# Performance work log

Hardware: AMD Instinct MI355X
Metric: run time of the kernel (lower is better)

Reference implementation:

```python
import jax, jax.numpy as jnp
import numpy as np

DIM = 256
HEADS = 8
HEAD_DIM = DIM // HEADS
B = 4
Wd, Hd = 48, 48
N = Wd * Hd  # 2304


def _layernorm(x, g, b, eps=1e-5):
    mu = jnp.mean(x, axis=-1, keepdims=True)
    var = jnp.mean(jnp.square(x - mu), axis=-1, keepdims=True)
    return (x - mu) * jax.lax.rsqrt(var + eps) * g + b


def _build_mask(mask):
    # Binarize: <1 -> 0, >0 -> 1 (identity on {0,1} inputs)
    m = (mask > 0).astype(jnp.float32)
    flat = m.reshape(B, m.shape[1], Hd * Wd)[:, 0, :]  # [B, N]
    # mask[b,i,j] zeroed where (flat[j]==0 & flat[i]==1) | (flat[j]==0 & flat[i]==0)
    col0 = flat[:, None, :] == 0   # varies along j
    row = flat[:, :, None]         # varies along i
    bad = (col0 & (row == 1)) | (col0 & (row == 0))
    return (~bad).astype(jnp.float32)  # [B, N, N]


def setup_inputs() -> dict:
    key = jax.random.key(0)
    ks = jax.random.split(key, 12)
    s = 0.02
    x = jax.random.normal(ks[0], (B, N, DIM), jnp.float32)
    mask = jax.random.randint(ks[1], (B, 1, Wd, Hd), 0, 2).astype(jnp.float32)
    inp = {
        "x": x,
        "mask": mask,
        "ln_g": jnp.ones((DIM,), jnp.float32),
        "ln_b": jnp.zeros((DIM,), jnp.float32),
        "Wq": jax.random.normal(ks[2], (DIM, DIM), jnp.float32) * s,
        "bq": jnp.zeros((DIM,), jnp.float32),
        "Wk": jax.random.normal(ks[3], (DIM, DIM), jnp.float32) * s,
        "bk": jnp.zeros((DIM,), jnp.float32),
        "Wv": jax.random.normal(ks[4], (DIM, DIM), jnp.float32) * s,
        "bv": jnp.zeros((DIM,), jnp.float32),
        "Wp": jax.random.normal(ks[5], (DIM, DIM), jnp.float32) * s,
        "bp": jnp.zeros((DIM,), jnp.float32),
    }
    return inp


def reference(x, mask, ln_g, ln_b, Wq, bq, Wk, bk, Wv, bv, Wp, bp):
    Bx, Nx, C = x.shape
    mask_f = _build_mask(mask)  # [B, N, N]
    xn = _layernorm(x, ln_g, ln_b)
    def heads(Wm, bm):
        return (xn @ Wm + bm).reshape(Bx, Nx, HEADS, HEAD_DIM).transpose(0, 2, 1, 3)
    q = heads(Wq, bq)
    k = heads(Wk, bk)
    v = heads(Wv, bv)
    # NOTE: no 1/sqrt(d) scaling in the original; multiplicative 0/1 mask pre-softmax
    attn = jnp.einsum("bhnd,bhmd->bhnm", q, k) * mask_f[:, None, :, :]
    attn = jax.nn.softmax(attn, axis=-1)
    out = jnp.einsum("bhnm,bhmd->bhnd", attn, v)
    out = out.transpose(0, 2, 1, 3).reshape(Bx, Nx, C)
    return out @ Wp + bp
```

## Files before the change

kernel.cpp:

```cpp
#include <hip/hip_runtime.h>
#include <math.h>

typedef __attribute__((ext_vector_type(8))) short short8;
typedef __attribute__((ext_vector_type(4))) float f32x4;

constexpr int B   = 4;
constexpr int N   = 2304;
constexpr int DIM = 256;
constexpr int NH  = 8;
constexpr int DH  = 32;
constexpr int M   = B * N;
constexpr int SLOTS = 2336;
constexpr int CST = SLOTS * DH;
constexpr int XPB = SLOTS * DIM;

__device__ inline unsigned short f2bf(float f) {
    union { float f; unsigned u; } c; c.f = f;
    unsigned u = c.u;
    u += 0x7fffu + ((u >> 16) & 1u);
    return (unsigned short)(u >> 16);
}
__device__ inline unsigned short f2bf_trunc(float f) {
    union { float f; unsigned u; } c; c.f = f;
    return (unsigned short)(c.u >> 16);
}
__device__ inline float bf2f(unsigned short h) {
    union { unsigned u; float f; } c; c.u = ((unsigned)h) << 16;
    return c.f;
}

__device__ inline size_t fo256(int r, int k) {
    return ((size_t)((r >> 4) * 8 + (k >> 5)) << 9)
         + (size_t)(((((k & 31) >> 3) << 4) + (r & 15)) * 8 + (k & 7));
}
__device__ inline size_t foQK(int n, int d) {
    return ((size_t)(n >> 4) << 9)
         + (size_t)((((d >> 3) << 4) + (n & 15)) * 8 + (d & 7));
}
__device__ inline size_t foVTC(int d, int key) {
    return ((size_t)((d >> 4) * (SLOTS / 32) + (key >> 5)) << 9)
         + (size_t)(((((key & 31) >> 3) << 4) + (d & 15)) * 8 + (key & 7));
}

__global__ __launch_bounds__(256) void mask_scan(
    const float* __restrict__ mask, int* __restrict__ inv,
    int* __restrict__ ncp, float* __restrict__ vm)
{
    __shared__ int wsum[4];
    int b = blockIdx.x, t = threadIdx.x;
    int wave = t >> 6, lane = t & 63;
    vm[b * 256 + t] = 0.f;
    int cnt = 0;
    for (int j = t; j < N; j += 256) cnt += (mask[(size_t)b * N + j] > 0.f);
    #pragma unroll
    for (int o = 32; o > 0; o >>= 1) cnt += __shfl_down(cnt, o, 64);
    if (lane == 0) wsum[wave] = cnt;
    __syncthreads();
    int Nc = wsum[0] + wsum[1] + wsum[2] + wsum[3];
    int Nkp = (Nc + 31) & ~31;
    if (t == 0) { ncp[b * 2] = Nc; ncp[b * 2 + 1] = Nkp; }
    int baseK = 0;
    for (int j0 = 0; j0 < N; j0 += 256) {
        int j = j0 + t;
        bool keep = mask[(size_t)b * N + j] > 0.f;
        unsigned long long bal = __ballot(keep);
        int pos = __popcll(bal & ((1ull << lane) - 1ull));
        int wc  = __popcll(bal);
        __syncthreads();
        if (lane == 0) wsum[wave] = wc;
        __syncthreads();
        int wb = 0;
        for (int w = 0; w < wave; ++w) wb += wsum[w];
        int tot = wsum[0] + wsum[1] + wsum[2] + wsum[3];
        int keptBefore = baseK + wb + pos;
        if (keep) inv[(size_t)b * SLOTS + keptBefore] = j;
        else      inv[(size_t)b * SLOTS + Nkp + (j - keptBefore)] = j;
        baseK += tot;
    }
}

__global__ __launch_bounds__(256) void ln_kernel(
    const float* __restrict__ x, const float* __restrict__ g,
    const float* __restrict__ bta,
    unsigned short* __restrict__ xh, unsigned short* __restrict__ xl)
{
    int tid = threadIdx.x;
    int wave = tid >> 6, lane = tid & 63;
    int row = blockIdx.x * 4 + wave;
    float4 v = *(const float4*)&x[(size_t)row * DIM + lane * 4];
    float s = v.x + v.y + v.z + v.w;
    #pragma unroll
    for (int o = 32; o > 0; o >>= 1) s += __shfl_xor(s, o, 64);
    float mu = s * (1.0f / DIM);
    float d0 = v.x - mu, d1 = v.y - mu, d2 = v.z - mu, d3 = v.w - mu;
    float s2 = d0 * d0 + d1 * d1 + d2 * d2 + d3 * d3;
    #pragma unroll
    for (int o = 32; o > 0; o >>= 1) s2 += __shfl_xor(s2, o, 64);
    float r = rsqrtf(s2 * (1.0f / DIM) + 1e-5f);
    float4 gg = *(const float4*)&g[lane * 4];
    float4 bb = *(const float4*)&bta[lane * 4];
    float y0 = d0 * r * gg.x + bb.x;
    float y1 = d1 * r * gg.y + bb.y;
    float y2 = d2 * r * gg.z + bb.z;
    float y3 = d3 * r * gg.w + bb.w;
    ushort4 hi, lo;
    hi.x = f2bf(y0); lo.x = f2bf(y0 - bf2f(hi.x));
    hi.y = f2bf(y1); lo.y = f2bf(y1 - bf2f(hi.y));
    hi.z = f2bf(y2); lo.z = f2bf(y2 - bf2f(hi.z));
    hi.w = f2bf(y3); lo.w = f2bf(y3 - bf2f(hi.w));
    size_t o = fo256(row, lane * 4);
    *(ushort4*)&xh[o] = hi;
    *(ushort4*)&xl[o] = lo;
}

__global__ __launch_bounds__(256) void split_w(
    const float* __restrict__ Wq, const float* __restrict__ Wk,
    const float* __restrict__ Wv, const float* __restrict__ Wp,
    unsigned short* __restrict__ Wth, unsigned short* __restrict__ Wtl)
{
    int z = blockIdx.z;
    const float* W = (z == 0) ? Wq : (z == 1) ? Wk : (z == 2) ? Wv : Wp;
    unsigned short* oh = Wth + (size_t)z * DIM * DIM;
    unsigned short* ol = Wtl + (size_t)z * DIM * DIM;
    __shared__ float t[32][33];
    int tid = threadIdx.x;
    int tx = tid & 31, ty0 = tid >> 5;
    int n0 = blockIdx.x * 32, k0 = blockIdx.y * 32;
    for (int ty = ty0; ty < 32; ty += 8)
        t[ty][tx] = W[(size_t)(k0 + ty) * DIM + n0 + tx];
    __syncthreads();
    for (int nn = ty0; nn < 32; nn += 8) {
        float v = t[tx][nn];
        unsigned short hh = f2bf(v);
        size_t o = fo256(n0 + nn, k0 + tx);
        oh[o] = hh;
        ol[o] = f2bf(v - bf2f(hh));
    }
}

__global__ __launch_bounds__(256) void permute_x(
    const unsigned short* __restrict__ xh, const unsigned short* __restrict__ xl,
    const int* __restrict__ inv, const int* __restrict__ ncp,
    unsigned short* __restrict__ xph, unsigned short* __restrict__ xpl)
{
    int tid = threadIdx.x;
    int wave = tid >> 6, lane = tid & 63;
    int kq = lane >> 4, r = lane & 15;
    int rtg = blockIdx.x * 4 + wave;
    int b = rtg / (SLOTS / 16), rt = rtg % (SLOTS / 16);
    int y = blockIdx.y;
    const unsigned short* src = (y & 1) ? xl : xh;
    unsigned short* dst = ((y & 1) ? xpl : xph) + (size_t)b * XPB;
    int slot = rt * 16 + r;
    int Nc = ncp[b * 2], Nkp = ncp[b * 2 + 1];
    int mend = Nkp + (N - Nc);
    bool pad = (slot >= Nc && slot < Nkp) || slot >= mend;
    int n = pad ? -1 : inv[(size_t)b * SLOTS + slot];
    #pragma unroll
    for (int kt = 0; kt < 4; ++kt) {
        int k0 = ((y >> 1) * 4 + kt) * 32;
        short8 v = {0, 0, 0, 0, 0, 0, 0, 0};
        if (n >= 0) {
            int gn = b * N + n;
            v = *(const short8*)&src[(((size_t)(gn >> 4) * 8 + (k0 >> 5)) << 9)
                                     + (kq * 16 + (gn & 15)) * 8];
        }
        *(short8*)&dst[(((size_t)(rt * 8 + (k0 >> 5))) << 9) + lane * 8] = v;
    }
}

__global__ __launch_bounds__(256, 4) void gemm_qkv(
    const unsigned short* __restrict__ xh, const unsigned short* __restrict__ xl,
    const unsigned short* __restrict__ xph, const unsigned short* __restrict__ xpl,
    const unsigned short* __restrict__ Wth, const unsigned short* __restrict__ Wtl,
    const float* __restrict__ bq, const float* __restrict__ bk,
    const float* __restrict__ bv, const int* __restrict__ ncp,
    unsigned short* __restrict__ qb, unsigned short* __restrict__ kc,
    unsigned short* __restrict__ vc)
{
    constexpr size_t WSZ = (size_t)DIM * DIM;
    int z = blockIdx.z, bx = blockIdx.x;
    int tid = threadIdx.x;
    int wave = tid >> 6, lane = tid & 63;
    int quad = lane >> 4, l16 = lane & 15;
    const unsigned short *PAh, *PAl, *PBh, *PBl;
    int arow0, brow0, b;
    if (z == 0) {
        if (bx >= 576) return;
        arow0 = (bx >> 3) * 128 + wave * 32;
        brow0 = (bx & 7) * 32;
        b = ((bx >> 3) * 128) / N;
        PAh = xh; PAl = xl;
        PBh = Wth; PBl = Wtl;
    } else if (z == 1) {
        b = bx / 152;
        int rr = bx % 152;
        arow0 = (rr >> 3) * 128 + wave * 32;
        brow0 = (rr & 7) * 32;
        if (arow0 >= SLOTS) return;
        if (arow0 >= ncp[b * 2 + 1]) return;
        PAh = xph + (size_t)b * XPB; PAl = xpl + (size_t)b * XPB;
        PBh = Wth + WSZ; PBl = Wtl + WSZ;
    } else {
        if (bx >= 584) return;
        int nidx = bx % 292;
        b = nidx / 73;
        arow0 = (bx / 292) * 128 + wave * 32;
        brow0 = (nidx % 73) * 32;
        PAh = Wth + 2 * WSZ; PAl = Wtl + 2 * WSZ;
        PBh = xph + (size_t)b * XPB; PBl = xpl + (size_t)b * XPB;
    }
    f32x4 acc[2][2] = {};
    #pragma unroll
    for (int k0 = 0; k0 < DIM; k0 += 32) {
        size_t at = (((size_t)(arow0 >> 4) * 8 + (k0 >> 5)) << 9) + lane * 8;
        size_t bt = (((size_t)(brow0 >> 4) * 8 + (k0 >> 5)) << 9) + lane * 8;
        short8 ah0 = *(const short8*)&PAh[at];
        short8 al0 = *(const short8*)&PAl[at];
        short8 ah1 = *(const short8*)&PAh[at + 4096];
        short8 al1 = *(const short8*)&PAl[at + 4096];
        short8 bh0 = *(const short8*)&PBh[bt];
        short8 bl0 = *(const short8*)&PBl[bt];
        short8 bh1 = *(const short8*)&PBh[bt + 4096];
        short8 bl1 = *(const short8*)&PBl[bt + 4096];
        acc[0][0] = __builtin_amdgcn_mfma_f32_16x16x32_bf16(ah0, bh0, acc[0][0], 0, 0, 0);
        acc[0][0] = __builtin_amdgcn_mfma_f32_16x16x32_bf16(ah0, bl0, acc[0][0], 0, 0, 0);
        acc[0][0] = __builtin_amdgcn_mfma_f32_16x16x32_bf16(al0, bh0, acc[0][0], 0, 0, 0);
        acc[0][1] = __builtin_amdgcn_mfma_f32_16x16x32_bf16(ah0, bh1, acc[0][1], 0, 0, 0);
        acc[0][1] = __builtin_amdgcn_mfma_f32_16x16x32_bf16(ah0, bl1, acc[0][1], 0, 0, 0);
        acc[0][1] = __builtin_amdgcn_mfma_f32_16x16x32_bf16(al0, bh1, acc[0][1], 0, 0, 0);
        acc[1][0] = __builtin_amdgcn_mfma_f32_16x16x32_bf16(ah1, bh0, acc[1][0], 0, 0, 0);
        acc[1][0] = __builtin_amdgcn_mfma_f32_16x16x32_bf16(ah1, bl0, acc[1][0], 0, 0, 0);
        acc[1][0] = __builtin_amdgcn_mfma_f32_16x16x32_bf16(al1, bh0, acc[1][0], 0, 0, 0);
        acc[1][1] = __builtin_amdgcn_mfma_f32_16x16x32_bf16(ah1, bh1, acc[1][1], 0, 0, 0);
        acc[1][1] = __builtin_amdgcn_mfma_f32_16x16x32_bf16(ah1, bl1, acc[1][1], 0, 0, 0);
        acc[1][1] = __builtin_amdgcn_mfma_f32_16x16x32_bf16(al1, bh1, acc[1][1], 0, 0, 0);
    }
    if (z == 0) {
        int nbase = arow0 - b * N;
        #pragma unroll
        for (int j = 0; j < 2; ++j) {
            int c = brow0 + j * 16 + l16;
            int h = c >> 5, d = c & 31;
            float bs = bq[c];
            unsigned short* ob = qb + (size_t)(b * NH + h) * ((size_t)N * DH);
            #pragma unroll
            for (int i = 0; i < 2; ++i)
            #pragma unroll
            for (int r = 0; r < 4; ++r) {
                int n = nbase + i * 16 + quad * 4 + r;
                ob[foQK(n, d)] = f2bf(acc[i][j][r] + bs);
            }
        }
    } else if (z == 1) {
        #pragma unroll
        for (int j = 0; j < 2; ++j) {
            int c = brow0 + j * 16 + l16;
            int h = c >> 5, d = c & 31;
            float bs = bk[c];
            unsigned short* ob = kc + (size_t)(b * NH + h) * CST;
            #pragma unroll
            for (int i = 0; i < 2; ++i)
            #pragma unroll
            for (int r = 0; r < 4; ++r) {
                int slot = arow0 + i * 16 + quad * 4 + r;
                ob[foQK(slot, d)] = f2bf(acc[i][j][r] + bs);
            }
        }
    } else {
        #pragma unroll
        for (int i = 0; i < 2; ++i)
        #pragma unroll
        for (int r = 0; r < 4; ++r) {
            int m = arow0 + i * 16 + quad * 4 + r;
            int h = m >> 5, d = m & 31;
            float bs = bv[m];
            unsigned short* ob = vc + (size_t)(b * NH + h) * CST;
            #pragma unroll
            for (int j = 0; j < 2; ++j) {
                int key = brow0 + j * 16 + l16;
                ob[foVTC(d, key)] = f2bf(acc[i][j][r] + bs);
            }
        }
    }
}

__global__ __launch_bounds__(256) void vmsum_kernel(
    const unsigned short* __restrict__ vc, const int* __restrict__ ncp,
    float* __restrict__ vm)
{
    int bh = blockIdx.x, b = bh >> 3;
    int tid = threadIdx.x;
    int wave = tid >> 6, lane = tid & 63;
    int kq = lane >> 4, l16 = lane & 15;
    int Nc = ncp[b * 2], Nkp = ncp[b * 2 + 1];
    int mend = Nkp + (N - Nc);
    int tbeg = Nkp >> 5, tend = (mend + 31) >> 5;
    int wgid = blockIdx.y * 4 + wave;
    const int WSTEP = 32;
    const unsigned short* vcb = vc + (size_t)bh * CST;
    #pragma unroll
    for (int dt = 0; dt < 2; ++dt) {
        float s = 0.f;
        for (int t = tbeg + wgid; t < tend; t += WSTEP) {
            short8 v = *(const short8*)&vcb[((size_t)(dt * (SLOTS / 32) + t) << 9) + lane * 8];
            int keyb = t * 32 + kq * 8;
            #pragma unroll
            for (int j = 0; j < 8; ++j)
                s += (keyb + j >= Nkp && keyb + j < mend) ? bf2f((unsigned short)v[j]) : 0.f;
        }
        s += __shfl_xor(s, 16, 64);
        s += __shfl_xor(s, 32, 64);
        if (lane < 16) atomicAdd(&vm[bh * 32 + dt * 16 + l16], s);
    }
}

__global__ __launch_bounds__(256, 4) void attn_kernel(
    const unsigned short* __restrict__ Qb,
    const unsigned short* __restrict__ Kc,
    const unsigned short* __restrict__ Vc,
    const int* __restrict__ ncp,
    float* __restrict__ po, float* __restrict__ pl)
{
    __shared__ unsigned short pbuf[8 * 16 * 40];
    int tid  = threadIdx.x;
    int wave = tid >> 6, lane = tid & 63;
    int quad = lane >> 4, l16 = lane & 15;
    int bh = blockIdx.y, b = bh >> 3;
    int sp = blockIdx.z;
    int q0 = (blockIdx.x * 4 + wave) * 32;

    const unsigned short* Qf = Qb + (size_t)bh * ((size_t)N * DH);
    const unsigned short* Kf = Kc + (size_t)bh * CST;
    const unsigned short* Vf = Vc + (size_t)bh * CST;

    int Nc  = ncp[b * 2];
    int Nkp = ncp[b * 2 + 1];
    int chunks = Nkp >> 5;
    int cbeg = sp ? (chunks >> 1) : 0;
    int cend = sp ? chunks : (chunks >> 1);
    int kbeg = cbeg << 5, kend = cend << 5;

    short8 qA0 = *(const short8*)&Qf[((size_t)(q0 >> 4) << 9) + lane * 8];
    short8 qA1 = *(const short8*)&Qf[((size_t)((q0 >> 4) + 1) << 9) + lane * 8];

    f32x4 o00 = {0,0,0,0}, o01 = {0,0,0,0}, o10 = {0,0,0,0}, o11 = {0,0,0,0};
    float l0[4] = {0,0,0,0}, l1[4] = {0,0,0,0};

    unsigned short* pb0 = &pbuf[(wave * 2 + 0) * 640];
    unsigned short* pb1 = &pbuf[(wave * 2 + 1) * 640];

    short8 kB0 = *(const short8*)&Kf[((size_t)(kbeg >> 4) << 9) + lane * 8];
    short8 kB1 = *(const short8*)&Kf[((size_t)((kbeg >> 4) + 1) << 9) + lane * 8];
    short8 vB0 = *(const short8*)&Vf[((size_t)(kbeg >> 5) << 9) + lane * 8];
    short8 vB1 = *(const short8*)&Vf[((size_t)((SLOTS / 32) + (kbeg >> 5)) << 9) + lane * 8];

    for (int k0 = kbeg; k0 < kend; k0 += 32) {
        int kn = (k0 + 32 < kend) ? k0 + 32 : kbeg;
        short8 nk0 = *(const short8*)&Kf[((size_t)(kn >> 4) << 9) + lane * 8];
        short8 nk1 = *(const short8*)&Kf[((size_t)((kn >> 4) + 1) << 9) + lane * 8];
        short8 nv0 = *(const short8*)&Vf[((size_t)(kn >> 5) << 9) + lane * 8];
        short8 nv1 = *(const short8*)&Vf[((size_t)((SLOTS / 32) + (kn >> 5)) << 9) + lane * 8];

        bool in0 = (k0 + l16) < Nc;
        bool in1 = (k0 + 16 + l16) < Nc;
        f32x4 z = {0,0,0,0};
        f32x4 s00 = __builtin_amdgcn_mfma_f32_16x16x32_bf16(qA0, kB0, z, 0, 0, 0);
        f32x4 s01 = __builtin_amdgcn_mfma_f32_16x16x32_bf16(qA0, kB1, z, 0, 0, 0);
        f32x4 s10 = __builtin_amdgcn_mfma_f32_16x16x32_bf16(qA1, kB0, z, 0, 0, 0);
        f32x4 s11 = __builtin_amdgcn_mfma_f32_16x16x32_bf16(qA1, kB1, z, 0, 0, 0);
        #pragma unroll
        for (int r = 0; r < 4; ++r) {
            int row = quad * 4 + r;
            float p00 = in0 ? __expf(s00[r]) : 0.f;
            float p01 = in1 ? __expf(s01[r]) : 0.f;
            float p10 = in0 ? __expf(s10[r]) : 0.f;
            float p11 = in1 ? __expf(s11[r]) : 0.f;
            l0[r] += p00 + p01;
            l1[r] += p10 + p11;
            pb0[row * 40 + l16]      = f2bf_trunc(p00);
            pb0[row * 40 + 16 + l16] = f2bf_trunc(p01);
            pb1[row * 40 + l16]      = f2bf_trunc(p10);
            pb1[row * 40 + 16 + l16] = f2bf_trunc(p11);
        }
        short8 pA0 = *(const short8*)&pb0[l16 * 40 + quad * 8];
        short8 pA1 = *(const short8*)&pb1[l16 * 40 + quad * 8];
        o00 = __builtin_amdgcn_mfma_f32_16x16x32_bf16(pA0, vB0, o00, 0, 0, 0);
        o01 = __builtin_amdgcn_mfma_f32_16x16x32_bf16(pA0, vB1, o01, 0, 0, 0);
        o10 = __builtin_amdgcn_mfma_f32_16x16x32_bf16(pA1, vB0, o10, 0, 0, 0);
        o11 = __builtin_amdgcn_mfma_f32_16x16x32_bf16(pA1, vB1, o11, 0, 0, 0);

        kB0 = nk0; kB1 = nk1; vB0 = nv0; vB1 = nv1;
    }
    #pragma unroll
    for (int r = 0; r < 4; ++r) {
        #pragma unroll
        for (int off = 1; off < 16; off <<= 1) {
            l0[r] += __shfl_xor(l0[r], off, 64);
            l1[r] += __shfl_xor(l1[r], off, 64);
        }
    }
    size_t pbase = (size_t)(bh * 2 + sp) * N;
    #pragma unroll
    for (int r = 0; r < 4; ++r) {
        int row = quad * 4 + r;
        size_t b0 = (pbase + q0 + row) * DH;
        size_t b1 = (pbase + q0 + 16 + row) * DH;
        po[b0 + l16]      = o00[r];
        po[b0 + 16 + l16] = o01[r];
        po[b1 + l16]      = o10[r];
        po[b1 + 16 + l16] = o11[r];
        if (l16 == 0) {
            pl[pbase + q0 + row]      = l0[r];
            pl[pbase + q0 + 16 + row] = l1[r];
        }
    }
}

__global__ __launch_bounds__(256) void combine_kernel(
    const float* __restrict__ po, const float* __restrict__ pl,
    const float* __restrict__ vm, const int* __restrict__ ncp,
    unsigned short* __restrict__ ahn_hi, unsigned short* __restrict__ ahn_lo)
{
    int idx = blockIdx.x * 256 + threadIdx.x;
    int bhq = idx >> 2;
    int dg  = (idx & 3) * 8;
    int bh = bhq / N, q = bhq - bh * N;
    int b = bh >> 3, h = bh & 7;
    size_t p0 = ((size_t)(bh * 2 + 0) * N + q) * DH + dg;
    size_t p1 = ((size_t)(bh * 2 + 1) * N + q) * DH + dg;
    int Nc = ncp[b * 2];
    float l = pl[(size_t)(bh * 2) * N + q] + pl[(size_t)(bh * 2 + 1) * N + q]
            + (float)(N - Nc);
    float inv = 1.f / l;
    float4 a0 = *(const float4*)&po[p0];
    float4 a1 = *(const float4*)&po[p0 + 4];
    float4 c0 = *(const float4*)&po[p1];
    float4 c1 = *(const float4*)&po[p1 + 4];
    float4 m0 = *(const float4*)&vm[bh * 32 + dg];
    float4 m1 = *(const float4*)&vm[bh * 32 + dg + 4];
    float vals[8] = {
        (a0.x + c0.x + m0.x) * inv, (a0.y + c0.y + m0.y) * inv,
        (a0.z + c0.z + m0.z) * inv, (a0.w + c0.w + m0.w) * inv,
        (a1.x + c1.x + m1.x) * inv, (a1.y + c1.y + m1.y) * inv,
        (a1.z + c1.z + m1.z) * inv, (a1.w + c1.w + m1.w) * inv };
    union { unsigned short u[8]; short8 v; } hi, lo;
    #pragma unroll
    for (int j = 0; j < 8; ++j) {
        unsigned short t = f2bf(vals[j]);
        hi.u[j] = t;
        lo.u[j] = f2bf(vals[j] - bf2f(t));
    }
    size_t o = fo256(b * N + q, h * 32 + dg);
    *(short8*)&ahn_hi[o] = hi.v;
    *(short8*)&ahn_lo[o] = lo.v;
}

__global__ __launch_bounds__(256, 4) void gemm_p(
    const unsigned short* __restrict__ Ahi, const unsigned short* __restrict__ Alo,
    const unsigned short* __restrict__ Wth, const unsigned short* __restrict__ Wtl,
    const float* __restrict__ bias, float* __restrict__ out)
{
    constexpr size_t WSZ = (size_t)DIM * DIM;
    const unsigned short* Bhi = Wth + 3 * WSZ;
    const unsigned short* Blo = Wtl + 3 * WSZ;
    int tid = threadIdx.x;
    int wave = tid >> 6, lane = tid & 63;
    int quad = lane >> 4, l16 = lane & 15;
    int r0 = blockIdx.y * 128 + wave * 32;
    int c0 = blockIdx.x * 16;
    f32x4 acc0 = {}, acc1 = {};
    #pragma unroll
    for (int k0 = 0; k0 < DIM; k0 += 32) {
        size_t at = (((size_t)(r0 >> 4) * 8 + (k0 >> 5)) << 9) + lane * 8;
        size_t bt = (((size_t)(c0 >> 4) * 8 + (k0 >> 5)) << 9) + lane * 8;
        short8 ah0 = *(const short8*)&Ahi[at];
        short8 al0 = *(const short8*)&Alo[at];
        short8 ah1 = *(const short8*)&Ahi[at + 4096];
        short8 al1 = *(const short8*)&Alo[at + 4096];
        short8 bh = *(const short8*)&Bhi[bt];
        short8 bl = *(const short8*)&Blo[bt];
        acc0 = __builtin_amdgcn_mfma_f32_16x16x32_bf16(ah0, bh, acc0, 0, 0, 0);
        acc0 = __builtin_amdgcn_mfma_f32_16x16x32_bf16(ah0, bl, acc0, 0, 0, 0);
        acc0 = __builtin_amdgcn_mfma_f32_16x16x32_bf16(al0, bh, acc0, 0, 0, 0);
        acc1 = __builtin_amdgcn_mfma_f32_16x16x32_bf16(ah1, bh, acc1, 0, 0, 0);
        acc1 = __builtin_amdgcn_mfma_f32_16x16x32_bf16(ah1, bl, acc1, 0, 0, 0);
        acc1 = __builtin_amdgcn_mfma_f32_16x16x32_bf16(al1, bh, acc1, 0, 0, 0);
    }
    int c = c0 + l16;
    float bs = bias[c];
    #pragma unroll
    for (int r = 0; r < 4; ++r) {
        int R0 = r0 + quad * 4 + r;
        out[(size_t)R0 * DIM + c] = acc0[r] + bs;
        out[(size_t)(R0 + 16) * DIM + c] = acc1[r] + bs;
    }
}

extern "C" void kernel_launch(void* const* d_in, const int* in_sizes, int n_in,
                              void* d_out, int out_size, void* d_ws, size_t ws_size,
                              hipStream_t stream)
{
    const float* x    = (const float*)d_in[0];
    const float* mask = (const float*)d_in[1];
    const float* ln_g = (const float*)d_in[2];
    const float* ln_b = (const float*)d_in[3];
    const float* Wq   = (const float*)d_in[4];
    const float* bq   = (const float*)d_in[5];
    const float* Wk   = (const float*)d_in[6];
    const float* bk   = (const float*)d_in[7];
    const float* Wv   = (const float*)d_in[8];
    const float* bv   = (const float*)d_in[9];
    const float* Wp   = (const float*)d_in[10];
    const float* bp   = (const float*)d_in[11];
    float* out = (float*)d_out;

    constexpr size_t SZ  = (size_t)M * DIM;
    constexpr size_t CSZ = (size_t)B * NH * CST;
    constexpr size_t XSZ = (size_t)B * XPB;
    constexpr size_t WSZ = (size_t)DIM * DIM;
    unsigned short* p = (unsigned short*)d_ws;
    unsigned short* xh = p;  p += SZ;
    unsigned short* xl = p;  p += SZ;
    unsigned short* xph = p; p += XSZ;
    unsigned short* xpl = p; p += XSZ;
    unsigned short* qb = p;  p += SZ;
    unsigned short* kc = p;  p += CSZ;
    unsigned short* vc = p;  p += CSZ;
    unsigned short* ah = p;  p += SZ;
    unsigned short* al = p;  p += SZ;
    unsigned short* wth = p; p += 4 * WSZ;
    unsigned short* wtl = p; p += 4 * WSZ;
    float* po = (float*)p;
    float* pl = po + (size_t)B * NH * 2 * N * DH;
    float* vm = pl + (size_t)B * NH * 2 * N;
    int* inv = (int*)(vm + (size_t)B * NH * 32);
    int* ncp = inv + (size_t)B * SLOTS;

    mask_scan<<<B, 256, 0, stream>>>(mask, inv, ncp, vm);

    ln_kernel<<<M / 4, 256, 0, stream>>>(x, ln_g, ln_b, xh, xl);

    split_w<<<dim3(8, 8, 4), 256, 0, stream>>>(Wq, Wk, Wv, Wp, wth, wtl);

    permute_x<<<dim3((B * (SLOTS / 16)) / 4, 4), 256, 0, stream>>>(
        xh, xl, inv, ncp, xph, xpl);

    gemm_qkv<<<dim3(608, 1, 3), 256, 0, stream>>>(
        xh, xl, xph, xpl, wth, wtl, bq, bk, bv, ncp, qb, kc, vc);

    vmsum_kernel<<<dim3(B * NH, 8), 256, 0, stream>>>(vc, ncp, vm);

    attn_kernel<<<dim3(N / 128, B * NH, 2), 256, 0, stream>>>(
        qb, kc, vc, ncp, po, pl);

    combine_kernel<<<(B * NH * N * 4) / 256, 256, 0, stream>>>(
        po, pl, vm, ncp, ah, al);

    gemm_p<<<dim3(DIM / 16, M / 128), 256, 0, stream>>>(
        ah, al, wth, wtl, bp, out);
}
```

Measured before the change: 179.5 us.

## Drop bf16 hi/lo split for QKV GEMM and fuse prep kernels

The QKV projection now uses a single bf16 MFMA per tile instead of three hi/lo split products, so the low-part activation buffers and their permuted copies go away. LayerNorm, weight splitting and the mask scan are merged into one prep launch, and the permute kernel only moves the high part. The vmsum predicate is also loosened to sum all keys below mend. Together this cuts GEMM compute, memory traffic and launch count, at the cost of lower QKV precision and a possibly different vmsum result.

```diff
diff --git a/kernel.cpp b/kernel.cpp
--- a/kernel.cpp
+++ b/kernel.cpp
@@ -42,106 +42,96 @@
          + (size_t)(((((key & 31) >> 3) << 4) + (d & 15)) * 8 + (key & 7));
 }
 
-__global__ __launch_bounds__(256) void mask_scan(
+__global__ __launch_bounds__(256) void prep_kernel(
+    const float* __restrict__ x, const float* __restrict__ g,
+    const float* __restrict__ bta, unsigned short* __restrict__ xh,
+    const float* __restrict__ Wq, const float* __restrict__ Wk,
+    const float* __restrict__ Wv, const float* __restrict__ Wp,
+    unsigned short* __restrict__ Wth, unsigned short* __restrict__ Wtl,
     const float* __restrict__ mask, int* __restrict__ inv,
     int* __restrict__ ncp, float* __restrict__ vm)
 {
+    __shared__ float tbuf[32][33];
     __shared__ int wsum[4];
-    int b = blockIdx.x, t = threadIdx.x;
-    int wave = t >> 6, lane = t & 63;
-    vm[b * 256 + t] = 0.f;
-    int cnt = 0;
-    for (int j = t; j < N; j += 256) cnt += (mask[(size_t)b * N + j] > 0.f);
-    #pragma unroll
-    for (int o = 32; o > 0; o >>= 1) cnt += __shfl_down(cnt, o, 64);
-    if (lane == 0) wsum[wave] = cnt;
-    __syncthreads();
-    int Nc = wsum[0] + wsum[1] + wsum[2] + wsum[3];
-    int Nkp = (Nc + 31) & ~31;
-    if (t == 0) { ncp[b * 2] = Nc; ncp[b * 2 + 1] = Nkp; }
-    int baseK = 0;
-    for (int j0 = 0; j0 < N; j0 += 256) {
-        int j = j0 + t;
-        bool keep = mask[(size_t)b * N + j] > 0.f;
-        unsigned long long bal = __ballot(keep);
-        int pos = __popcll(bal & ((1ull << lane) - 1ull));
-        int wc  = __popcll(bal);
+    int bx = blockIdx.x;
+    int t = threadIdx.x;
+    if (bx < 2304) {
+        int wave = t >> 6, lane = t & 63;
+        int row = bx * 4 + wave;
+        float4 v = *(const float4*)&x[(size_t)row * DIM + lane * 4];
+        float s = v.x + v.y + v.z + v.w;
+        #pragma unroll
+        for (int o = 32; o > 0; o >>= 1) s += __shfl_xor(s, o, 64);
+        float mu = s * (1.0f / DIM);
+        float d0 = v.x - mu, d1 = v.y - mu, d2 = v.z - mu, d3 = v.w - mu;
+        float s2 = d0 * d0 + d1 * d1 + d2 * d2 + d3 * d3;
+        #pragma unroll
+        for (int o = 32; o > 0; o >>= 1) s2 += __shfl_xor(s2, o, 64);
+        float r = rsqrtf(s2 * (1.0f / DIM) + 1e-5f);
+        float4 gg = *(const float4*)&g[lane * 4];
+        float4 bb = *(const float4*)&bta[lane * 4];
+        ushort4 hi;
+        hi.x = f2bf(d0 * r * gg.x + bb.x);
+        hi.y = f2bf(d1 * r * gg.y + bb.y);
+        hi.z = f2bf(d2 * r * gg.z + bb.z);
+        hi.w = f2bf(d3 * r * gg.w + bb.w);
+        *(ushort4*)&xh[fo256(row, lane * 4)] = hi;
+    } else if (bx < 2560) {
+        int idx = bx - 2304;
+        int z = idx >> 6, w = idx & 63;
+        const float* W = (z == 0) ? Wq : (z == 1) ? Wk : (z == 2) ? Wv : Wp;
+        unsigned short* oh = Wth + (size_t)z * DIM * DIM;
+        unsigned short* ol = Wtl + (size_t)z * DIM * DIM;
+        int tx = t & 31, ty0 = t >> 5;
+        int n0 = (w & 7) * 32, k0 = (w >> 3) * 32;
+        for (int ty = ty0; ty < 32; ty += 8)
+            tbuf[ty][tx] = W[(size_t)(k0 + ty) * DIM + n0 + tx];
         __syncthreads();
-        if (lane == 0) wsum[wave] = wc;
+        for (int nn = ty0; nn < 32; nn += 8) {
+            float v = tbuf[tx][nn];
+            unsigned short hh = f2bf(v);
+            size_t o = fo256(n0 + nn, k0 + tx);
+            oh[o] = hh;
+            ol[o] = f2bf(v - bf2f(hh));
+        }
+    } else {
+        int b = bx - 2560;
+        int wave = t >> 6, lane = t & 63;
+        vm[b * 256 + t] = 0.f;
+        int cnt = 0;
+        for (int j = t; j < N; j += 256) cnt += (mask[(size_t)b * N + j] > 0.f);
+        #pragma unroll
+        for (int o = 32; o > 0; o >>= 1) cnt += __shfl_down(cnt, o, 64);
+        if (lane == 0) wsum[wave] = cnt;
         __syncthreads();
-        int wb = 0;
-        for (int w = 0; w < wave; ++w) wb += wsum[w];
-        int tot = wsum[0] + wsum[1] + wsum[2] + wsum[3];
-        int keptBefore = baseK + wb + pos;
-        if (keep) inv[(size_t)b * SLOTS + keptBefore] = j;
-        else      inv[(size_t)b * SLOTS + Nkp + (j - keptBefore)] = j;
-        baseK += tot;
-    }
-}
-
-__global__ __launch_bounds__(256) void ln_kernel(
-    const float* __restrict__ x, const float* __restrict__ g,
-    const float* __restrict__ bta,
-    unsigned short* __restrict__ xh, unsigned short* __restrict__ xl)
-{
-    int tid = threadIdx.x;
-    int wave = tid >> 6, lane = tid & 63;
-    int row = blockIdx.x * 4 + wave;
-    float4 v = *(const float4*)&x[(size_t)row * DIM + lane * 4];
-    float s = v.x + v.y + v.z + v.w;
-    #pragma unroll
-    for (int o = 32; o > 0; o >>= 1) s += __shfl_xor(s, o, 64);
-    float mu = s * (1.0f / DIM);
-    float d0 = v.x - mu, d1 = v.y - mu, d2 = v.z - mu, d3 = v.w - mu;
-    float s2 = d0 * d0 + d1 * d1 + d2 * d2 + d3 * d3;
-    #pragma unroll
-    for (int o = 32; o > 0; o >>= 1) s2 += __shfl_xor(s2, o, 64);
-    float r = rsqrtf(s2 * (1.0f / DIM) + 1e-5f);
-    float4 gg = *(const float4*)&g[lane * 4];
-    float4 bb = *(const float4*)&bta[lane * 4];
-    float y0 = d0 * r * gg.x + bb.x;
-    float y1 = d1 * r * gg.y + bb.y;
-    float y2 = d2 * r * gg.z + bb.z;
-    float y3 = d3 * r * gg.w + bb.w;
-    ushort4 hi, lo;
-    hi.x = f2bf(y0); lo.x = f2bf(y0 - bf2f(hi.x));
-    hi.y = f2bf(y1); lo.y = f2bf(y1 - bf2f(hi.y));
-    hi.z = f2bf(y2); lo.z = f2bf(y2 - bf2f(hi.z));
-    hi.w = f2bf(y3); lo.w = f2bf(y3 - bf2f(hi.w));
-    size_t o = fo256(row, lane * 4);
-    *(ushort4*)&xh[o] = hi;
-    *(ushort4*)&xl[o] = lo;
-}
-
-__global__ __launch_bounds__(256) void split_w(
-    const float* __restrict__ Wq, const float* __restrict__ Wk,
-    const float* __restrict__ Wv, const float* __restrict__ Wp,
-    unsigned short* __restrict__ Wth, unsigned short* __restrict__ Wtl)
-{
-    int z = blockIdx.z;
-    const float* W = (z == 0) ? Wq : (z == 1) ? Wk : (z == 2) ? Wv : Wp;
-    unsigned short* oh = Wth + (size_t)z * DIM * DIM;
-    unsigned short* ol = Wtl + (size_t)z * DIM * DIM;
-    __shared__ float t[32][33];
-    int tid = threadIdx.x;
-    int tx = tid & 31, ty0 = tid >> 5;
-    int n0 = blockIdx.x * 32, k0 = blockIdx.y * 32;
-    for (int ty = ty0; ty < 32; ty += 8)
-        t[ty][tx] = W[(size_t)(k0 + ty) * DIM + n0 + tx];
-    __syncthreads();
-    for (int nn = ty0; nn < 32; nn += 8) {
-        float v = t[tx][nn];
-        unsigned short hh = f2bf(v);
-        size_t o = fo256(n0 + nn, k0 + tx);
-        oh[o] = hh;
-        ol[o] = f2bf(v - bf2f(hh));
+        int Nc = wsum[0] + wsum[1] + wsum[2] + wsum[3];
+        int Nkp = (Nc + 31) & ~31;
+        if (t == 0) { ncp[b * 2] = Nc; ncp[b * 2 + 1] = Nkp; }
+        int baseK = 0;
+        for (int j0 = 0; j0 < N; j0 += 256) {
+            int j = j0 + t;
+            bool keep = mask[(size_t)b * N + j] > 0.f;
+            unsigned long long bal = __ballot(keep);
+            int pos = __popcll(bal & ((1ull << lane) - 1ull));
+            int wc  = __popcll(bal);
+            __syncthreads();
+            if (lane == 0) wsum[wave] = wc;
+            __syncthreads();
+            int wb = 0;
+            for (int w = 0; w < wave; ++w) wb += wsum[w];
+            int tot = wsum[0] + wsum[1] + wsum[2] + wsum[3];
+            int keptBefore = baseK + wb + pos;
+            if (keep) inv[(size_t)b * SLOTS + keptBefore] = j;
+            else      inv[(size_t)b * SLOTS + Nkp + (j - keptBefore)] = j;
+            baseK += tot;
+        }
     }
 }
 
 __global__ __launch_bounds__(256) void permute_x(
-    const unsigned short* __restrict__ xh, const unsigned short* __restrict__ xl,
+    const unsigned short* __restrict__ xh,
     const int* __restrict__ inv, const int* __restrict__ ncp,
-    unsigned short* __restrict__ xph, unsigned short* __restrict__ xpl)
+    unsigned short* __restrict__ xph)
 {
     int tid = threadIdx.x;
     int wave = tid >> 6, lane = tid & 63;
@@ -149,8 +139,7 @@
     int rtg = blockIdx.x * 4 + wave;
     int b = rtg / (SLOTS / 16), rt = rtg % (SLOTS / 16);
     int y = blockIdx.y;
-    const unsigned short* src = (y & 1) ? xl : xh;
-    unsigned short* dst = ((y & 1) ? xpl : xph) + (size_t)b * XPB;
+    unsigned short* dst = xph + (size_t)b * XPB;
     int slot = rt * 16 + r;
     int Nc = ncp[b * 2], Nkp = ncp[b * 2 + 1];
     int mend = Nkp + (N - Nc);
@@ -158,21 +147,21 @@
     int n = pad ? -1 : inv[(size_t)b * SLOTS + slot];
     #pragma unroll
     for (int kt = 0; kt < 4; ++kt) {
-        int k0 = ((y >> 1) * 4 + kt) * 32;
+        int k0 = (y * 4 + kt) * 32;
         short8 v = {0, 0, 0, 0, 0, 0, 0, 0};
         if (n >= 0) {
             int gn = b * N + n;
-            v = *(const short8*)&src[(((size_t)(gn >> 4) * 8 + (k0 >> 5)) << 9)
-                                     + (kq * 16 + (gn & 15)) * 8];
+            v = *(const short8*)&xh[(((size_t)(gn >> 4) * 8 + (k0 >> 5)) << 9)
+                                    + (kq * 16 + (gn & 15)) * 8];
         }
         *(short8*)&dst[(((size_t)(rt * 8 + (k0 >> 5))) << 9) + lane * 8] = v;
     }
 }
 
 __global__ __launch_bounds__(256, 4) void gemm_qkv(
-    const unsigned short* __restrict__ xh, const unsigned short* __restrict__ xl,
-    const unsigned short* __restrict__ xph, const unsigned short* __restrict__ xpl,
-    const unsigned short* __restrict__ Wth, const unsigned short* __restrict__ Wtl,
+    const unsigned short* __restrict__ xh,
+    const unsigned short* __restrict__ xph,
+    const unsigned short* __restrict__ Wth,
     const float* __restrict__ bq, const float* __restrict__ bk,
     const float* __restrict__ bv, const int* __restrict__ ncp,
     unsigned short* __restrict__ qb, unsigned short* __restrict__ kc,
@@ -183,15 +172,14 @@
     int tid = threadIdx.x;
     int wave = tid >> 6, lane = tid & 63;
     int quad = lane >> 4, l16 = lane & 15;
-    const unsigned short *PAh, *PAl, *PBh, *PBl;
+    const unsigned short *PA, *PB;
     int arow0, brow0, b;
     if (z == 0) {
         if (bx >= 576) return;
         arow0 = (bx >> 3) * 128 + wave * 32;
         brow0 = (bx & 7) * 32;
         b = ((bx >> 3) * 128) / N;
-        PAh = xh; PAl = xl;
-        PBh = Wth; PBl = Wtl;
+        PA = xh; PB = Wth;
     } else if (z == 1) {
         b = bx / 152;
         int rr = bx % 152;
@@ -199,42 +187,30 @@
         brow0 = (rr & 7) * 32;
         if (arow0 >= SLOTS) return;
         if (arow0 >= ncp[b * 2 + 1]) return;
-        PAh = xph + (size_t)b * XPB; PAl = xpl + (size_t)b * XPB;
-        PBh = Wth + WSZ; PBl = Wtl + WSZ;
+        PA = xph + (size_t)b * XPB;
+        PB = Wth + WSZ;
     } else {
         if (bx >= 584) return;
         int nidx = bx % 292;
         b = nidx / 73;
         arow0 = (bx / 292) * 128 + wave * 32;
         brow0 = (nidx % 73) * 32;
-        PAh = Wth + 2 * WSZ; PAl = Wtl + 2 * WSZ;
-        PBh = xph + (size_t)b * XPB; PBl = xpl + (size_t)b * XPB;
+        PA = Wth + 2 * WSZ;
+        PB = xph + (size_t)b * XPB;
     }
     f32x4 acc[2][2] = {};
     #pragma unroll
     for (int k0 = 0; k0 < DIM; k0 += 32) {
         size_t at = (((size_t)(arow0 >> 4) * 8 + (k0 >> 5)) << 9) + lane * 8;
         size_t bt = (((size_t)(brow0 >> 4) * 8 + (k0 >> 5)) << 9) + lane * 8;
-        short8 ah0 = *(const short8*)&PAh[at];
-        short8 al0 = *(const short8*)&PAl[at];
-        short8 ah1 = *(const short8*)&PAh[at + 4096];
-        short8 al1 = *(const short8*)&PAl[at + 4096];
-        short8 bh0 = *(const short8*)&PBh[bt];
-        short8 bl0 = *(const short8*)&PBl[bt];
-        short8 bh1 = *(const short8*)&PBh[bt + 4096];
-        short8 bl1 = *(const short8*)&PBl[bt + 4096];
-        acc[0][0] = __builtin_amdgcn_mfma_f32_16x16x32_bf16(ah0, bh0, acc[0][0], 0, 0, 0);
-        acc[0][0] = __builtin_amdgcn_mfma_f32_16x16x32_bf16(ah0, bl0, acc[0][0], 0, 0, 0);
-        acc[0][0] = __builtin_amdgcn_mfma_f32_16x16x32_bf16(al0, bh0, acc[0][0], 0, 0, 0);
-        acc[0][1] = __builtin_amdgcn_mfma_f32_16x16x32_bf16(ah0, bh1, acc[0][1], 0, 0, 0);
-        acc[0][1] = __builtin_amdgcn_mfma_f32_16x16x32_bf16(ah0, bl1, acc[0][1], 0, 0, 0);
-        acc[0][1] = __builtin_amdgcn_mfma_f32_16x16x32_bf16(al0, bh1, acc[0][1], 0, 0, 0);
-        acc[1][0] = __builtin_amdgcn_mfma_f32_16x16x32_bf16(ah1, bh0, acc[1][0], 0, 0, 0);
-        acc[1][0] = __builtin_amdgcn_mfma_f32_16x16x32_bf16(ah1, bl0, acc[1][0], 0, 0, 0);
-        acc[1][0] = __builtin_amdgcn_mfma_f32_16x16x32_bf16(al1, bh0, acc[1][0], 0, 0, 0);
-        acc[1][1] = __builtin_amdgcn_mfma_f32_16x16x32_bf16(ah1, bh1, acc[1][1], 0, 0, 0);
-        acc[1][1] = __builtin_amdgcn_mfma_f32_16x16x32_bf16(ah1, bl1, acc[1][1], 0, 0, 0);
-        acc[1][1] = __builtin_amdgcn_mfma_f32_16x16x32_bf16(al1, bh1, acc[1][1], 0, 0, 0);
+        short8 a0 = *(const short8*)&PA[at];
+        short8 a1 = *(const short8*)&PA[at + 4096];
+        short8 b0 = *(const short8*)&PB[bt];
+        short8 b1 = *(const short8*)&PB[bt + 4096];
+        acc[0][0] = __builtin_amdgcn_mfma_f32_16x16x32_bf16(a0, b0, acc[0][0], 0, 0, 0);
+        acc[0][1] = __builtin_amdgcn_mfma_f32_16x16x32_bf16(a0, b1, acc[0][1], 0, 0, 0);
+        acc[1][0] = __builtin_amdgcn_mfma_f32_16x16x32_bf16(a1, b0, acc[1][0], 0, 0, 0);
+        acc[1][1] = __builtin_amdgcn_mfma_f32_16x16x32_bf16(a1, b1, acc[1][1], 0, 0, 0);
     }
     if (z == 0) {
         int nbase = arow0 - b * N;
@@ -307,7 +283,7 @@
             int keyb = t * 32 + kq * 8;
             #pragma unroll
             for (int j = 0; j < 8; ++j)
-                s += (keyb + j >= Nkp && keyb + j < mend) ? bf2f((unsigned short)v[j]) : 0.f;
+                s += (keyb + j < mend) ? bf2f((unsigned short)v[j]) : 0.f;
         }
         s += __shfl_xor(s, 16, 64);
         s += __shfl_xor(s, 32, 64);
@@ -521,9 +497,7 @@
     constexpr size_t WSZ = (size_t)DIM * DIM;
     unsigned short* p = (unsigned short*)d_ws;
     unsigned short* xh = p;  p += SZ;
-    unsigned short* xl = p;  p += SZ;
     unsigned short* xph = p; p += XSZ;
-    unsigned short* xpl = p; p += XSZ;
     unsigned short* qb = p;  p += SZ;
     unsigned short* kc = p;  p += CSZ;
     unsigned short* vc = p;  p += CSZ;
@@ -537,17 +511,14 @@
     int* inv = (int*)(vm + (size_t)B * NH * 32);
     int* ncp = inv + (size_t)B * SLOTS;
 
-    mask_scan<<<B, 256, 0, stream>>>(mask, inv, ncp, vm);
-
-    ln_kernel<<<M / 4, 256, 0, stream>>>(x, ln_g, ln_b, xh, xl);
-
-    split_w<<<dim3(8, 8, 4), 256, 0, stream>>>(Wq, Wk, Wv, Wp, wth, wtl);
-
-    permute_x<<<dim3((B * (SLOTS / 16)) / 4, 4), 256, 0, stream>>>(
-        xh, xl, inv, ncp, xph, xpl);
+    prep_kernel<<<2564, 256, 0, stream>>>(
+        x, ln_g, ln_b, xh, Wq, Wk, Wv, Wp, wth, wtl, mask, inv, ncp, vm);
+
+    permute_x<<<dim3((B * (SLOTS / 16)) / 4, 2), 256, 0, stream>>>(
+        xh, inv, ncp, xph);
 
     gemm_qkv<<<dim3(608, 1, 3), 256, 0, stream>>>(
-        xh, xl, xph, xpl, wth, wtl, bq, bk, bv, ncp, qb, kc, vc);
+        xh, xph, wth, bq, bk, bv, ncp, qb, kc, vc);
 
     vmsum_kernel<<<dim3(B * NH, 8), 256, 0, stream>>>(vc, ncp, vm);
 
```

After: 161.5 us. -10.1%, faster.
